# Performance work log

Measured on AMD Instinct MI355X. Metric: run time of the kernel, lower is better.

## Reference

```python
import jax, jax.numpy as jnp
import numpy as np

# Hyperparameters from init_kwargs
LAMBDA_VAL = 5.0
MARGIN = 0.02
INTERCLASS_COEF = 0.5
HIGH_CONSTANT = 2.0
EPS = 1e-5


def _rank(seq):
    # torch: argsort(argsort(seq).flip(-1)) -> rank 0 for the largest element
    idx = jnp.flip(jnp.argsort(seq, axis=-1), axis=-1)
    return jnp.argsort(idx, axis=-1)


def rank_normalised(seq):
    n = seq.shape[-1]
    return (_rank(seq) + 1).astype(seq.dtype) / n


@jax.custom_vjp
def true_ranker(seq):
    # Blackbox-differentiable ranking (TrueRanker.apply)
    return rank_normalised(seq)


def _tr_fwd(seq):
    r = rank_normalised(seq)
    return r, (seq, r)


def _tr_bwd(res, g):
    seq, r = res
    r_prime = rank_normalised(seq + LAMBDA_VAL * g)
    return (-(r - r_prime) / (LAMBDA_VAL + 1e-8),)


true_ranker.defvjp(_tr_fwd, _tr_bwd)


def raw_map(scores, targets, key):
    """scores/targets: [N, C]. Faithful port of MapLoss.raw_map_computation."""
    ts = scores.T  # [C, N]
    tt = targets.T  # [C, N]
    # random margin deviations: pushed down for positives, up for negatives
    dev = jnp.abs(jax.random.normal(key, tt.shape, tt.dtype)) * (tt - 0.5)
    ts = ts - MARGIN * dev
    ranks_of_positive = true_ranker(ts)  # [C, N], normalized ranks in (0,1]
    scores_for_rp = -ranks_of_positive + HIGH_CONSTANT * tt
    # torch sets requires_grad=False on this rank -> stop_gradient
    ranks_within_positive = jax.lax.stop_gradient(rank_normalised(scores_for_rp))
    sum_prec = (ranks_within_positive / ranks_of_positive * tt).sum(axis=1)  # [C]
    prec = sum_prec / (tt.sum(axis=1) + EPS)  # [C]
    present = targets.sum(axis=0) != 0  # [C]
    denom = jnp.maximum(jnp.sum(present), 1).astype(prec.dtype)
    return 1.0 - jnp.sum(jnp.where(present, prec, 0.0)) / denom


def setup_inputs() -> dict:
    key = jax.random.key(0)
    k1, k2, k3, k4 = jax.random.split(key, 4)
    B, C, M = 256, 8192, 4
    P_POS = 0.01  # sparse binary relevance labels
    output = jax.random.normal(k1, (B, C), jnp.float32)
    target = (jax.random.uniform(k2, (B, C)) < P_POS).astype(jnp.float32)
    stored_output = jax.random.normal(k3, (M * B, C), jnp.float32)
    stored_target = (jax.random.uniform(k4, (M * B, C)) < P_POS).astype(jnp.float32)
    return {"output": output, "target": target,
            "stored_output": stored_output, "stored_target": stored_target}


def reference(output, target, stored_output, stored_target):
    # storage entries were detach()'d in torch -> stop_gradient
    long_out = jnp.concatenate([output, jax.lax.stop_gradient(stored_output)], axis=0)
    long_tgt = jnp.concatenate([target, stored_target], axis=0)
    k_cross, k_inter = jax.random.split(jax.random.key(42))
    cross_batch_loss = raw_map(long_out, long_tgt, k_cross)
    interclass_loss = raw_map(output.reshape(-1, 1), target.reshape(-1, 1), k_inter)
    return (1.0 - INTERCLASS_COEF) * cross_batch_loss + INTERCLASS_COEF * interclass_loss
```

## Files before the change

kernel.cpp:

```cpp
#include <hip/hip_runtime.h>
#include <stdint.h>

#define USE_PARTITIONABLE 1

#define C_CLASSES 8192
#define N_ROWS 1280
#define HALF_CROSS (C_CLASSES * N_ROWS / 2)
#define N_INTER 2097152
#define HALF_INTER (N_INTER / 2)
#define PCAP 32768
#define NB (1u << 20)
#define BSHIFT 12
#define IPB 2048
#define PPB 96
#define CNT_CAP 24576
#define CNT_WORDS (CNT_CAP / 4)
#define KE_BLOCKS 256
#define KE_ELEMS (N_INTER / KE_BLOCKS)
#define CPB 16

__host__ __device__ __forceinline__ void tf2x32(unsigned k0, unsigned k1,
                                                unsigned c0, unsigned c1,
                                                unsigned& o0, unsigned& o1) {
  const unsigned ks2 = k0 ^ k1 ^ 0x1BD11BDAu;
  unsigned x0 = c0 + k0, x1 = c1 + k1;
#define TF_R(r) { x0 += x1; x1 = (x1 << (r)) | (x1 >> (32 - (r))); x1 ^= x0; }
  TF_R(13) TF_R(15) TF_R(26) TF_R(6)   x0 += k1;  x1 += ks2 + 1u;
  TF_R(17) TF_R(29) TF_R(16) TF_R(24)  x0 += ks2; x1 += k0 + 2u;
  TF_R(13) TF_R(15) TF_R(26) TF_R(6)   x0 += k0;  x1 += k1 + 3u;
  TF_R(17) TF_R(29) TF_R(16) TF_R(24)  x0 += k1;  x1 += ks2 + 4u;
  TF_R(13) TF_R(15) TF_R(26) TF_R(6)   x0 += ks2; x1 += k0 + 5u;
#undef TF_R
  o0 = x0; o1 = x1;
}

__device__ __forceinline__ unsigned rand_bits(unsigned k0, unsigned k1,
                                              unsigned p, unsigned half) {
#if USE_PARTITIONABLE
  (void)half;
  unsigned a, b; tf2x32(k0, k1, 0u, p, a, b);
  return a ^ b;
#else
  unsigned c0 = (p < half) ? p : (p - half);
  unsigned a, b; tf2x32(k0, k1, c0, c0 + half, a, b);
  return (p < half) ? a : b;
#endif
}

__device__ __forceinline__ float erfinv_xla(float x) {
  float w = -log1pf(-x * x);
  float p;
  if (w < 5.0f) {
    w = w - 2.5f;
    p = 2.81022636e-08f;
    p = fmaf(p, w, 3.43273939e-07f);
    p = fmaf(p, w, -3.5233877e-06f);
    p = fmaf(p, w, -4.39150654e-06f);
    p = fmaf(p, w, 0.00021858087f);
    p = fmaf(p, w, -0.00125372503f);
    p = fmaf(p, w, -0.00417768164f);
    p = fmaf(p, w, 0.246640727f);
    p = fmaf(p, w, 1.50140941f);
  } else {
    w = sqrtf(w) - 3.0f;
    p = -0.000200214257f;
    p = fmaf(p, w, 0.000100950558f);
    p = fmaf(p, w, 0.00134934322f);
    p = fmaf(p, w, -0.00367342844f);
    p = fmaf(p, w, 0.00573950773f);
    p = fmaf(p, w, -0.0076224613f);
    p = fmaf(p, w, 0.00943887047f);
    p = fmaf(p, w, 1.00167406f);
    p = fmaf(p, w, 2.83297682f);
  }
  return p * x;
}

__device__ __forceinline__ float normal_from_bits(unsigned bits) {
  unsigned fb = (bits >> 9) | 0x3F800000u;
  float f = __uint_as_float(fb) - 1.0f;
  float u = fmaxf(-0.99999994f, f * 2.0f - 0.99999994f);
  return 1.41421356f * erfinv_xla(u);
}

__device__ __forceinline__ unsigned sortable_key(float sp) {
  unsigned b = __float_as_uint(sp);
  return (b & 0x80000000u) ? ~b : (b | 0x80000000u);
}

__global__ void __launch_bounds__(1024) kcross_fused(
    const float* __restrict__ outp, const float* __restrict__ tgt,
    const float* __restrict__ soutp, const float* __restrict__ stgt,
    float* __restrict__ prec_arr, float* __restrict__ pres_arr,
    unsigned k0, unsigned k1) {
  __shared__ float skey[N_ROWS][CPB + 1];
  __shared__ unsigned tmask[N_ROWS];
  __shared__ unsigned short plist[CPB][64];
  __shared__ int pcnt[CPB];
  __shared__ unsigned rankl[CPB][64];
  const int tid = threadIdx.x;
  const int c0 = blockIdx.x * CPB;

  for (int i = tid; i < N_ROWS; i += 1024) tmask[i] = 0u;
  if (tid < CPB) pcnt[tid] = 0;
  __syncthreads();

#pragma unroll
  for (int i = 0; i < 5; ++i) {
    int f = i * 1024 + tid;
    int n = f >> 2, quad = f & 3;
    const float* tp = (n < 256) ? (tgt + (size_t)n * C_CLASSES)
                                : (stgt + (size_t)(n - 256) * C_CLASSES);
    float4 tv = *(const float4*)(tp + c0 + quad * 4);
    unsigned nib = (tv.x != 0.f ? 1u : 0u) | (tv.y != 0.f ? 2u : 0u) |
                   (tv.z != 0.f ? 4u : 0u) | (tv.w != 0.f ? 8u : 0u);
    if (nib) {
      atomicOr(&tmask[n], nib << (quad * 4));
#pragma unroll
      for (int k = 0; k < 4; ++k) {
        if (nib & (1u << k)) {
          int j = quad * 4 + k;
          int slot = atomicAdd(&pcnt[j], 1);
          if (slot < 64) plist[j][slot] = (unsigned short)n;
        }
      }
    }
  }
  __syncthreads();

#pragma unroll
  for (int i = 0; i < 5; ++i) {
    int f = i * 1024 + tid;
    int n = f >> 2, quad = f & 3;
    const float* sp_ = (n < 256) ? (outp + (size_t)n * C_CLASSES)
                                 : (soutp + (size_t)(n - 256) * C_CLASSES);
    float4 sv = *(const float4*)(sp_ + c0 + quad * 4);
    unsigned tm = tmask[n];
    float r[4] = {sv.x, sv.y, sv.z, sv.w};
#pragma unroll
    for (int k = 0; k < 4; ++k) {
      int j = quad * 4 + k;
      unsigned p = (unsigned)((c0 + j) * N_ROWS + n);
      float nrm = normal_from_bits(rand_bits(k0, k1, p, HALF_CROSS));
      float tvf = ((tm >> j) & 1u) ? 1.0f : 0.0f;
      r[k] = r[k] - 0.02f * (fabsf(nrm) * (tvf - 0.5f));
      skey[n][j] = r[k];
    }
  }
  __syncthreads();

  const int j = tid >> 6;
  const int lane = tid & 63;
  const int P = pcnt[j] < 64 ? pcnt[j] : 64;
  for (int pi = 0; pi < P; ++pi) {
    int ip = plist[j][pi];
    float spv = skey[ip][j];
    int cnt = 0;
#pragma unroll
    for (int s = 0; s < 20; ++s) {
      int n = lane + 64 * s;
      float x = skey[n][j];
      cnt += (x > spv) || ((x == spv) & (n > ip));
    }
    cnt += __shfl_down(cnt, 32);
    cnt += __shfl_down(cnt, 16);
    cnt += __shfl_down(cnt, 8);
    cnt += __shfl_down(cnt, 4);
    cnt += __shfl_down(cnt, 2);
    cnt += __shfl_down(cnt, 1);
    if (lane == 0) rankl[j][pi] = (unsigned)cnt;
  }
  double acc = 0.0;
  if (lane < P) {
    int ip = plist[j][lane];
    float spv = skey[ip][j];
    int k = 1;
    for (int q = 0; q < P; ++q) {
      int iq = plist[j][q];
      float sq = skey[iq][j];
      k += (sq > spv) || ((sq == spv) & (iq > ip));
    }
    unsigned rr = rankl[j][lane];
    float rw = (float)k / 1280.0f;
    float ro = (float)(rr + 1u) / 1280.0f;
    acc = (double)(rw / ro);
  }
#pragma unroll
  for (int o = 32; o; o >>= 1) acc += __shfl_down(acc, o);
  if (lane == 0) {
    if (P > 0) {
      float sum_prec = (float)acc;
      prec_arr[c0 + j] = sum_prec / ((float)P + 1e-5f);
      pres_arr[c0 + j] = 1.0f;
    } else {
      prec_arr[c0 + j] = 0.0f;
      pres_arr[c0 + j] = 0.0f;
    }
  }
}

__global__ void kinter_prep(const float* __restrict__ outp, const float* __restrict__ tgt,
                            unsigned* __restrict__ ukey,
                            unsigned long long* __restrict__ pk64_tmp,
                            unsigned* __restrict__ blockCnt,
                            unsigned* __restrict__ hist_pos,
                            unsigned k0, unsigned k1) {
  __shared__ unsigned scnt;
  if (threadIdx.x == 0) scnt = 0;
  __syncthreads();
  const int blk = blockIdx.x;
#pragma unroll
  for (int i = 0; i < 4; ++i) {
    int n = blk * 1024 + i * 256 + threadIdx.x;
    float t = tgt[n], sv = outp[n];
    float nrm = normal_from_bits(rand_bits(k0, k1, (unsigned)n, HALF_INTER));
    float sp = sv - 0.02f * (fabsf(nrm) * (t - 0.5f));
    unsigned key = sortable_key(sp);
    ukey[n] = key;
    if (t != 0.0f) {
      unsigned slot = atomicAdd(&scnt, 1u);
      if (slot < PPB) {
        pk64_tmp[(size_t)blk * PPB + slot] = ((unsigned long long)key << 21) | (unsigned)n;
        atomicAdd(&hist_pos[key >> BSHIFT], 1u);
      }
    }
  }
  __syncthreads();
  if (threadIdx.x == 0) blockCnt[blk] = scnt < PPB ? scnt : PPB;
}

__global__ void kscan1(const unsigned* __restrict__ hist_pos, unsigned* __restrict__ chunkSum) {
  __shared__ unsigned ls[256];
  const int t = threadIdx.x;
  uint4 v = ((const uint4*)(hist_pos + (size_t)blockIdx.x * 1024))[t];
  ls[t] = v.x + v.y + v.z + v.w;
  __syncthreads();
  for (int o = 128; o; o >>= 1) { if (t < o) ls[t] += ls[t + o]; __syncthreads(); }
  if (t == 0) chunkSum[blockIdx.x] = ls[0];
}

__global__ void kscan2(const unsigned* __restrict__ chunkSum, unsigned* __restrict__ chunkPre,
                       const unsigned* __restrict__ blockCnt, unsigned* pcount) {
  __shared__ unsigned ls[1024];
  const int t = threadIdx.x;
  unsigned own = chunkSum[t];
  ls[t] = own;
  __syncthreads();
  for (int off = 1; off < 1024; off <<= 1) {
    unsigned v = (t >= off) ? ls[t - off] : 0u;
    __syncthreads();
    ls[t] += v;
    __syncthreads();
  }
  chunkPre[t] = ls[t] - own;
  __syncthreads();
  unsigned s = blockCnt[t] + blockCnt[t + 1024];
  ls[t] = s;
  __syncthreads();
  for (int o = 512; o; o >>= 1) { if (t < o) ls[t] += ls[t + o]; __syncthreads(); }
  if (t == 0) *pcount = ls[0];
}

__global__ void kscan3(const unsigned* __restrict__ hist_pos, const unsigned* __restrict__ chunkPre,
                       unsigned* __restrict__ cursor, unsigned* __restrict__ bsh) {
  __shared__ unsigned ls[256];
  const int t = threadIdx.x;
  uint4 v = ((const uint4*)(hist_pos + (size_t)blockIdx.x * 1024))[t];
  unsigned tsum = v.x + v.y + v.z + v.w;
  ls[t] = tsum;
  __syncthreads();
  for (int off = 1; off < 256; off <<= 1) {
    unsigned u = (t >= off) ? ls[t - off] : 0u;
    __syncthreads();
    ls[t] += u;
    __syncthreads();
  }
  unsigned base = chunkPre[blockIdx.x] + ls[t] - tsum;
  uint4 cu; cu.x = base; cu.y = base + v.x; cu.z = cu.y + v.y; cu.w = cu.z + v.z;
  ((uint4*)cursor)[blockIdx.x * 256 + t] = cu;
  uint4 bs;
  bs.x = (cu.x << 8) | (v.x > 255u ? 255u : v.x);
  bs.y = (cu.y << 8) | (v.y > 255u ? 255u : v.y);
  bs.z = (cu.z << 8) | (v.z > 255u ? 255u : v.z);
  bs.w = (cu.w << 8) | (v.w > 255u ? 255u : v.w);
  ((uint4*)bsh)[blockIdx.x * 256 + t] = bs;
}

__global__ void kpos_scatter(const unsigned long long* __restrict__ pk64_tmp,
                             const unsigned* __restrict__ blockCnt,
                             unsigned* cursor, unsigned long long* __restrict__ t64) {
  unsigned j = blockIdx.x * 256 + threadIdx.x;
  unsigned b = j / PPB, i = j % PPB;
  if (i >= blockCnt[b]) return;
  unsigned long long k64 = pk64_tmp[j];
  unsigned bkt = (unsigned)(k64 >> 33);
  unsigned slot = atomicAdd(&cursor[bkt], 1u);
  t64[slot] = k64;
}

__global__ void kpos_fix(const unsigned long long* __restrict__ t64,
                         const unsigned* __restrict__ hist_pos,
                         const unsigned* __restrict__ cursor,
                         const unsigned* pcount, unsigned long long* __restrict__ spk64) {
  unsigned j = blockIdx.x * 256 + threadIdx.x;
  unsigned P = *pcount;
  if (j >= P) return;
  unsigned long long my = t64[j];
  unsigned bkt = (unsigned)(my >> 33);
  unsigned hp = hist_pos[bkt];
  unsigned start = cursor[bkt] - hp;
  unsigned lt = 0;
  if (hp > 1) {
    for (unsigned m = start; m < start + hp; ++m) lt += (t64[m] < my);
  }
  spk64[start + lt] = my;
}

__global__ void __launch_bounds__(1024) kelem2(
    const unsigned* __restrict__ ukey, const unsigned* __restrict__ bsh,
    const unsigned long long* __restrict__ spk64,
    unsigned* __restrict__ cnt_blocks) {
  __shared__ unsigned cntp[CNT_WORDS];
  const int tid = threadIdx.x;
  for (int i = tid; i < CNT_WORDS; i += 1024) cntp[i] = 0;
  __syncthreads();
#pragma unroll
  for (int it = 0; it < 8; ++it) {
    int n = blockIdx.x * KE_ELEMS + it * 1024 + tid;
    unsigned key = ukey[n];
    unsigned long long k64 = ((unsigned long long)key << 21) | (unsigned)n;
    unsigned info = bsh[key >> BSHIFT];
    unsigned cntLess = info >> 8;
    unsigned hp = info & 0xFFu;
    if (hp) {
      unsigned start = cntLess;
      for (unsigned m = start; m < start + hp; ++m) cntLess += (spk64[m] < k64);
    }
    if (cntLess > CNT_CAP - 1) cntLess = CNT_CAP - 1;
    atomicAdd(&cntp[cntLess >> 2], 1u << ((cntLess & 3u) * 8u));
  }
  __syncthreads();
  unsigned* dst = cnt_blocks + (size_t)blockIdx.x * CNT_WORDS;
  for (int i = tid; i < CNT_WORDS; i += 1024) dst[i] = cntp[i];
}

__global__ void kreduce(const unsigned* __restrict__ cnt_blocks, unsigned* __restrict__ tot) {
  unsigned i = blockIdx.x * 256 + threadIdx.x;
  unsigned s0 = 0, s1 = 0, s2 = 0, s3 = 0;
  for (int b = 0; b < KE_BLOCKS; ++b) {
    unsigned v = cnt_blocks[(size_t)b * CNT_WORDS + i];
    s0 += v & 0xFFu; s1 += (v >> 8) & 0xFFu; s2 += (v >> 16) & 0xFFu; s3 += v >> 24;
  }
  tot[4 * i] = s0; tot[4 * i + 1] = s1; tot[4 * i + 2] = s2; tot[4 * i + 3] = s3;
}

__global__ void __launch_bounds__(1024) kfinal(
    const float* __restrict__ prec_arr, const float* __restrict__ pres_arr,
    const unsigned* __restrict__ tot, const unsigned* pcount, float* __restrict__ out) {
  __shared__ double rd[1024];
  __shared__ unsigned lsum[1024];
  const int t = threadIdx.x;
  const unsigned P = *pcount;
  const int CH = CNT_CAP / 1024;
  unsigned lv[CH];
  unsigned mys = 0;
#pragma unroll
  for (int i = 0; i < CH; ++i) { lv[i] = tot[t * CH + i]; mys += lv[i]; }
  lsum[t] = mys;
  __syncthreads();
  for (int off = 1; off < 1024; off <<= 1) {
    unsigned v = (t + off < 1024) ? lsum[t + off] : 0u;
    __syncthreads();
    lsum[t] += v;
    __syncthreads();
  }
  unsigned run = (t < 1023) ? lsum[t + 1] : 0u;
  double acc = 0.0;
#pragma unroll
  for (int i = CH - 1; i >= 0; --i) {
    unsigned idx = (unsigned)(t * CH + i);
    unsigned r = run;
    if (idx < P) acc += (double)((float)(P - idx) / (float)(r + 1u));
    run += lv[i];
  }
  rd[t] = acc;
  __syncthreads();
  for (int o = 512; o; o >>= 1) { if (t < o) rd[t] += rd[t + o]; __syncthreads(); }
  double interSum = rd[0];
  __syncthreads();
  double a = 0.0, bb = 0.0;
  for (int i = t; i < C_CLASSES; i += 1024) { a += (double)prec_arr[i]; bb += (double)pres_arr[i]; }
  rd[t] = a;
  __syncthreads();
  for (int o = 512; o; o >>= 1) { if (t < o) rd[t] += rd[t + o]; __syncthreads(); }
  double crossSum = rd[0];
  __syncthreads();
  rd[t] = bb;
  __syncthreads();
  for (int o = 512; o; o >>= 1) { if (t < o) rd[t] += rd[t + o]; __syncthreads(); }
  if (t == 0) {
    float pc = (float)rd[0];
    float denomC = pc > 0.0f ? pc : 1.0f;
    float crossLoss = 1.0f - (float)crossSum / denomC;
    float interPrec = (float)interSum / ((float)P + 1e-5f);
    float interLoss = 1.0f - interPrec;
    out[0] = 0.5f * crossLoss + 0.5f * interLoss;
  }
}

extern "C" void kernel_launch(void* const* d_in, const int* in_sizes, int n_in,
                              void* d_out, int out_size, void* d_ws, size_t ws_size,
                              hipStream_t stream) {
  (void)in_sizes; (void)n_in; (void)out_size; (void)ws_size;
  const float* outp  = (const float*)d_in[0];
  const float* tgt   = (const float*)d_in[1];
  const float* soutp = (const float*)d_in[2];
  const float* stgt  = (const float*)d_in[3];
  float* dst = (float*)d_out;

  unsigned ck0, ck1, ik0, ik1;
#if USE_PARTITIONABLE
  tf2x32(0u, 42u, 0u, 0u, ck0, ck1);
  tf2x32(0u, 42u, 0u, 1u, ik0, ik1);
#else
  { unsigned a0, b0, a1, b1;
    tf2x32(0u, 42u, 0u, 2u, a0, b0);
    tf2x32(0u, 42u, 1u, 3u, a1, b1);
    ck0 = a0; ck1 = a1; ik0 = b0; ik1 = b1; }
#endif

  uint8_t* w = (uint8_t*)d_ws;
  size_t o = 0;
  unsigned* hist_pos   = (unsigned*)(w + o); o += (size_t)NB * 4;
  unsigned* cursor     = (unsigned*)(w + o); o += (size_t)NB * 4;
  unsigned* bsh        = (unsigned*)(w + o); o += (size_t)NB * 4;
  unsigned* ukey       = (unsigned*)(w + o); o += (size_t)N_INTER * 4;
  unsigned* chunkSum   = (unsigned*)(w + o); o += 1024 * 4;
  unsigned* chunkPre   = (unsigned*)(w + o); o += 1024 * 4;
  unsigned long long* pk64_tmp = (unsigned long long*)(w + o); o += (size_t)IPB * PPB * 8;
  unsigned* blockCnt   = (unsigned*)(w + o); o += (size_t)IPB * 4;
  unsigned long long* t64   = (unsigned long long*)(w + o); o += (size_t)PCAP * 8;
  unsigned long long* spk64 = (unsigned long long*)(w + o); o += (size_t)PCAP * 8;
  unsigned* cnt_blocks = (unsigned*)(w + o); o += (size_t)KE_BLOCKS * CNT_WORDS * 4;
  unsigned* tot        = (unsigned*)(w + o); o += (size_t)CNT_CAP * 4;
  float*    prec_arr   = (float*)(w + o);    o += (size_t)C_CLASSES * 4;
  float*    pres_arr   = (float*)(w + o);    o += (size_t)C_CLASSES * 4;
  unsigned* pcount     = (unsigned*)(w + o); o += 64;

  hipMemsetAsync(hist_pos, 0, (size_t)NB * 4, stream);

  kcross_fused<<<C_CLASSES / CPB, 1024, 0, stream>>>(
      outp, tgt, soutp, stgt, prec_arr, pres_arr, ck0, ck1);
  kinter_prep<<<IPB, 256, 0, stream>>>(outp, tgt, ukey, pk64_tmp, blockCnt, hist_pos, ik0, ik1);
  kscan1<<<NB / 1024, 256, 0, stream>>>(hist_pos, chunkSum);
  kscan2<<<1, 1024, 0, stream>>>(chunkSum, chunkPre, blockCnt, pcount);
  kscan3<<<NB / 1024, 256, 0, stream>>>(hist_pos, chunkPre, cursor, bsh);
  kpos_scatter<<<IPB * PPB / 256, 256, 0, stream>>>(pk64_tmp, blockCnt, cursor, t64);
  kpos_fix<<<PCAP / 256, 256, 0, stream>>>(t64, hist_pos, cursor, pcount, spk64);
  kelem2<<<KE_BLOCKS, 1024, 0, stream>>>(ukey, bsh, spk64, cnt_blocks);
  kreduce<<<CNT_WORDS / 256, 256, 0, stream>>>(cnt_blocks, tot);
  kfinal<<<1, 1024, 0, stream>>>(prec_arr, pres_arr, tot, pcount, dst);
}
```

Baseline: 271.1 us.

## Fuse interclass pipeline into one cooperative kernel and retune cross-batch ranking

```diff
diff --git a/kernel.cpp b/kernel.cpp
--- a/kernel.cpp
+++ b/kernel.cpp
@@ -1,5 +1,8 @@
 #include <hip/hip_runtime.h>
+#include <hip/hip_cooperative_groups.h>
 #include <stdint.h>
+
+namespace cg = cooperative_groups;
 
 #define USE_PARTITIONABLE 1
 
@@ -8,16 +11,19 @@
 #define HALF_CROSS (C_CLASSES * N_ROWS / 2)
 #define N_INTER 2097152
 #define HALF_INTER (N_INTER / 2)
-#define PCAP 32768
 #define NB (1u << 20)
 #define BSHIFT 12
-#define IPB 2048
-#define PPB 96
 #define CNT_CAP 24576
 #define CNT_WORDS (CNT_CAP / 4)
-#define KE_BLOCKS 256
-#define KE_ELEMS (N_INTER / KE_BLOCKS)
-#define CPB 16
+#define CPB 8
+
+#define MBLK 256
+#define MTHR 1024
+#define EPB (N_INTER / MBLK)
+#define EPT (EPB / MTHR)
+#define PLOC 192
+#define BPB ((int)(NB / MBLK))
+#define WPB (CNT_WORDS / MBLK)
 
 __host__ __device__ __forceinline__ void tf2x32(unsigned k0, unsigned k1,
                                                 unsigned c0, unsigned c1,
@@ -88,38 +94,38 @@
   return (b & 0x80000000u) ? ~b : (b | 0x80000000u);
 }
 
-__global__ void __launch_bounds__(1024) kcross_fused(
+__global__ void __launch_bounds__(512, 6) kcross_fused(
     const float* __restrict__ outp, const float* __restrict__ tgt,
     const float* __restrict__ soutp, const float* __restrict__ stgt,
     float* __restrict__ prec_arr, float* __restrict__ pres_arr,
     unsigned k0, unsigned k1) {
   __shared__ float skey[N_ROWS][CPB + 1];
-  __shared__ unsigned tmask[N_ROWS];
+  __shared__ unsigned tmask32[N_ROWS / 4];
   __shared__ unsigned short plist[CPB][64];
   __shared__ int pcnt[CPB];
-  __shared__ unsigned rankl[CPB][64];
+  __shared__ unsigned short rankl[CPB][64];
   const int tid = threadIdx.x;
   const int c0 = blockIdx.x * CPB;
 
-  for (int i = tid; i < N_ROWS; i += 1024) tmask[i] = 0u;
+  for (int i = tid; i < N_ROWS / 4; i += 512) tmask32[i] = 0u;
   if (tid < CPB) pcnt[tid] = 0;
   __syncthreads();
 
 #pragma unroll
   for (int i = 0; i < 5; ++i) {
-    int f = i * 1024 + tid;
-    int n = f >> 2, quad = f & 3;
+    int f = i * 512 + tid;
+    int n = f >> 1, half = f & 1;
     const float* tp = (n < 256) ? (tgt + (size_t)n * C_CLASSES)
                                 : (stgt + (size_t)(n - 256) * C_CLASSES);
-    float4 tv = *(const float4*)(tp + c0 + quad * 4);
+    float4 tv = *(const float4*)(tp + c0 + half * 4);
     unsigned nib = (tv.x != 0.f ? 1u : 0u) | (tv.y != 0.f ? 2u : 0u) |
                    (tv.z != 0.f ? 4u : 0u) | (tv.w != 0.f ? 8u : 0u);
     if (nib) {
-      atomicOr(&tmask[n], nib << (quad * 4));
+      atomicOr(&tmask32[n >> 2], nib << ((n & 3) * 8 + half * 4));
 #pragma unroll
       for (int k = 0; k < 4; ++k) {
         if (nib & (1u << k)) {
-          int j = quad * 4 + k;
+          int j = half * 4 + k;
           int slot = atomicAdd(&pcnt[j], 1);
           if (slot < 64) plist[j][slot] = (unsigned short)n;
         }
@@ -130,205 +136,193 @@
 
 #pragma unroll
   for (int i = 0; i < 5; ++i) {
-    int f = i * 1024 + tid;
-    int n = f >> 2, quad = f & 3;
+    int f = i * 512 + tid;
+    int n = f >> 1, half = f & 1;
     const float* sp_ = (n < 256) ? (outp + (size_t)n * C_CLASSES)
                                  : (soutp + (size_t)(n - 256) * C_CLASSES);
-    float4 sv = *(const float4*)(sp_ + c0 + quad * 4);
-    unsigned tm = tmask[n];
-    float r[4] = {sv.x, sv.y, sv.z, sv.w};
+    float4 sv = *(const float4*)(sp_ + c0 + half * 4);
+    unsigned tmr = tmask32[n >> 2] >> ((n & 3) * 8);
+    float vals[4] = {sv.x, sv.y, sv.z, sv.w};
 #pragma unroll
     for (int k = 0; k < 4; ++k) {
-      int j = quad * 4 + k;
+      int j = half * 4 + k;
       unsigned p = (unsigned)((c0 + j) * N_ROWS + n);
       float nrm = normal_from_bits(rand_bits(k0, k1, p, HALF_CROSS));
-      float tvf = ((tm >> j) & 1u) ? 1.0f : 0.0f;
-      r[k] = r[k] - 0.02f * (fabsf(nrm) * (tvf - 0.5f));
-      skey[n][j] = r[k];
-    }
-  }
-  __syncthreads();
-
-  const int j = tid >> 6;
-  const int lane = tid & 63;
-  const int P = pcnt[j] < 64 ? pcnt[j] : 64;
-  for (int pi = 0; pi < P; ++pi) {
-    int ip = plist[j][pi];
-    float spv = skey[ip][j];
-    int cnt = 0;
-#pragma unroll
+      float tvf = ((tmr >> j) & 1u) ? 1.0f : 0.0f;
+      skey[n][j] = vals[k] - 0.02f * (fabsf(nrm) * (tvf - 0.5f));
+    }
+  }
+  __syncthreads();
+
+  const int j = tid >> 6, lane = tid & 63;
+  int P = pcnt[j]; if (P > 64) P = 64;
+  for (int base = 0; base < P; base += 8) {
+    float spv[8]; int ipv[8];
+#pragma unroll
+    for (int k = 0; k < 8; ++k) {
+      int pi = base + k;
+      if (pi < P) { ipv[k] = plist[j][pi]; spv[k] = skey[ipv[k]][j]; }
+      else { ipv[k] = 0x7fffffff; spv[k] = __int_as_float(0x7f800000); }
+    }
+    unsigned c16[4] = {0u, 0u, 0u, 0u};
     for (int s = 0; s < 20; ++s) {
-      int n = lane + 64 * s;
+      int n = lane + (s << 6);
       float x = skey[n][j];
-      cnt += (x > spv) || ((x == spv) & (n > ip));
-    }
-    cnt += __shfl_down(cnt, 32);
-    cnt += __shfl_down(cnt, 16);
-    cnt += __shfl_down(cnt, 8);
-    cnt += __shfl_down(cnt, 4);
-    cnt += __shfl_down(cnt, 2);
-    cnt += __shfl_down(cnt, 1);
-    if (lane == 0) rankl[j][pi] = (unsigned)cnt;
+#pragma unroll
+      for (int k = 0; k < 8; ++k) {
+        unsigned bb = (x > spv[k]) || ((x == spv[k]) & (n > ipv[k]));
+        c16[k >> 1] += bb << ((k & 1) * 16);
+      }
+    }
+#pragma unroll
+    for (int q = 0; q < 4; ++q) {
+      unsigned v = c16[q];
+      v += __shfl_down(v, 32); v += __shfl_down(v, 16); v += __shfl_down(v, 8);
+      v += __shfl_down(v, 4);  v += __shfl_down(v, 2);  v += __shfl_down(v, 1);
+      if (lane == 0) {
+        int p0 = base + 2 * q;
+        if (p0 < P)     rankl[j][p0]     = (unsigned short)(v & 0xFFFFu);
+        if (p0 + 1 < P) rankl[j][p0 + 1] = (unsigned short)(v >> 16);
+      }
+    }
   }
   double acc = 0.0;
   if (lane < P) {
     int ip = plist[j][lane];
-    float spv = skey[ip][j];
-    int k = 1;
+    float spv0 = skey[ip][j];
+    int kk = 1;
     for (int q = 0; q < P; ++q) {
       int iq = plist[j][q];
       float sq = skey[iq][j];
-      k += (sq > spv) || ((sq == spv) & (iq > ip));
+      kk += (sq > spv0) || ((sq == spv0) & (iq > ip));
     }
     unsigned rr = rankl[j][lane];
-    float rw = (float)k / 1280.0f;
+    float rw = (float)kk / 1280.0f;
     float ro = (float)(rr + 1u) / 1280.0f;
     acc = (double)(rw / ro);
   }
 #pragma unroll
   for (int o = 32; o; o >>= 1) acc += __shfl_down(acc, o);
   if (lane == 0) {
-    if (P > 0) {
-      float sum_prec = (float)acc;
-      prec_arr[c0 + j] = sum_prec / ((float)P + 1e-5f);
-      pres_arr[c0 + j] = 1.0f;
-    } else {
-      prec_arr[c0 + j] = 0.0f;
-      pres_arr[c0 + j] = 0.0f;
-    }
-  }
-}
-
-__global__ void kinter_prep(const float* __restrict__ outp, const float* __restrict__ tgt,
-                            unsigned* __restrict__ ukey,
-                            unsigned long long* __restrict__ pk64_tmp,
-                            unsigned* __restrict__ blockCnt,
-                            unsigned* __restrict__ hist_pos,
-                            unsigned k0, unsigned k1) {
-  __shared__ unsigned scnt;
-  if (threadIdx.x == 0) scnt = 0;
-  __syncthreads();
-  const int blk = blockIdx.x;
-#pragma unroll
-  for (int i = 0; i < 4; ++i) {
-    int n = blk * 1024 + i * 256 + threadIdx.x;
+    if (P > 0) { prec_arr[c0 + j] = (float)acc / ((float)P + 1e-5f); pres_arr[c0 + j] = 1.0f; }
+    else       { prec_arr[c0 + j] = 0.0f;                            pres_arr[c0 + j] = 0.0f; }
+  }
+}
+
+__global__ void __launch_bounds__(1024) kinter_mega(
+    const float* __restrict__ outp, const float* __restrict__ tgt,
+    unsigned* __restrict__ hist_pos, unsigned* __restrict__ cursor,
+    unsigned* __restrict__ bsh, unsigned* __restrict__ chunkTot,
+    unsigned long long* __restrict__ t64, unsigned long long* __restrict__ spk64,
+    unsigned* __restrict__ cnt_blocks, unsigned* __restrict__ tot,
+    const float* __restrict__ prec_arr, const float* __restrict__ pres_arr,
+    float* __restrict__ out, unsigned k0, unsigned k1) {
+  cg::grid_group grid = cg::this_grid();
+  __shared__ unsigned lkey[EPB];
+  __shared__ unsigned cntp[CNT_WORDS];
+  __shared__ unsigned sc[MTHR];
+  __shared__ unsigned long long pk_loc[PLOC];
+  __shared__ int scnt;
+  __shared__ unsigned uP;
+  __shared__ double rd[1024];
+  __shared__ unsigned lsum[1024];
+  const int tid = threadIdx.x;
+  const int b = blockIdx.x;
+
+  if (tid == 0) scnt = 0;
+  __syncthreads();
+
+#pragma unroll
+  for (int it = 0; it < EPT; ++it) {
+    int loc = it * MTHR + tid;
+    int n = b * EPB + loc;
     float t = tgt[n], sv = outp[n];
     float nrm = normal_from_bits(rand_bits(k0, k1, (unsigned)n, HALF_INTER));
     float sp = sv - 0.02f * (fabsf(nrm) * (t - 0.5f));
     unsigned key = sortable_key(sp);
-    ukey[n] = key;
+    lkey[loc] = key;
     if (t != 0.0f) {
-      unsigned slot = atomicAdd(&scnt, 1u);
-      if (slot < PPB) {
-        pk64_tmp[(size_t)blk * PPB + slot] = ((unsigned long long)key << 21) | (unsigned)n;
+      int slot = atomicAdd(&scnt, 1);
+      if (slot < PLOC) {
+        pk_loc[slot] = ((unsigned long long)key << 21) | (unsigned)n;
         atomicAdd(&hist_pos[key >> BSHIFT], 1u);
       }
     }
   }
-  __syncthreads();
-  if (threadIdx.x == 0) blockCnt[blk] = scnt < PPB ? scnt : PPB;
-}
-
-__global__ void kscan1(const unsigned* __restrict__ hist_pos, unsigned* __restrict__ chunkSum) {
-  __shared__ unsigned ls[256];
-  const int t = threadIdx.x;
-  uint4 v = ((const uint4*)(hist_pos + (size_t)blockIdx.x * 1024))[t];
-  ls[t] = v.x + v.y + v.z + v.w;
-  __syncthreads();
-  for (int o = 128; o; o >>= 1) { if (t < o) ls[t] += ls[t + o]; __syncthreads(); }
-  if (t == 0) chunkSum[blockIdx.x] = ls[0];
-}
-
-__global__ void kscan2(const unsigned* __restrict__ chunkSum, unsigned* __restrict__ chunkPre,
-                       const unsigned* __restrict__ blockCnt, unsigned* pcount) {
-  __shared__ unsigned ls[1024];
-  const int t = threadIdx.x;
-  unsigned own = chunkSum[t];
-  ls[t] = own;
-  __syncthreads();
-  for (int off = 1; off < 1024; off <<= 1) {
-    unsigned v = (t >= off) ? ls[t - off] : 0u;
-    __syncthreads();
-    ls[t] += v;
-    __syncthreads();
-  }
-  chunkPre[t] = ls[t] - own;
-  __syncthreads();
-  unsigned s = blockCnt[t] + blockCnt[t + 1024];
-  ls[t] = s;
-  __syncthreads();
-  for (int o = 512; o; o >>= 1) { if (t < o) ls[t] += ls[t + o]; __syncthreads(); }
-  if (t == 0) *pcount = ls[0];
-}
-
-__global__ void kscan3(const unsigned* __restrict__ hist_pos, const unsigned* __restrict__ chunkPre,
-                       unsigned* __restrict__ cursor, unsigned* __restrict__ bsh) {
-  __shared__ unsigned ls[256];
-  const int t = threadIdx.x;
-  uint4 v = ((const uint4*)(hist_pos + (size_t)blockIdx.x * 1024))[t];
-  unsigned tsum = v.x + v.y + v.z + v.w;
-  ls[t] = tsum;
-  __syncthreads();
-  for (int off = 1; off < 256; off <<= 1) {
-    unsigned u = (t >= off) ? ls[t - off] : 0u;
-    __syncthreads();
-    ls[t] += u;
-    __syncthreads();
-  }
-  unsigned base = chunkPre[blockIdx.x] + ls[t] - tsum;
-  uint4 cu; cu.x = base; cu.y = base + v.x; cu.z = cu.y + v.y; cu.w = cu.z + v.z;
-  ((uint4*)cursor)[blockIdx.x * 256 + t] = cu;
+  grid.sync();
+
+  uint4 hv = ((const uint4*)(hist_pos + (size_t)b * BPB))[tid];
+  unsigned tsum = hv.x + hv.y + hv.z + hv.w;
+  sc[tid] = tsum;
+  __syncthreads();
+  for (int off = 1; off < MTHR; off <<= 1) {
+    unsigned v = (tid >= off) ? sc[tid - off] : 0u;
+    __syncthreads();
+    sc[tid] += v;
+    __syncthreads();
+  }
+  unsigned pre_t = sc[tid] - tsum;
+  if (tid == MTHR - 1) chunkTot[b] = sc[tid];
+  grid.sync();
+
+  if (tid < MBLK) sc[tid] = chunkTot[tid];
+  __syncthreads();
+  for (int off = 1; off < MBLK; off <<= 1) {
+    unsigned v = (tid < MBLK && tid >= off) ? sc[tid - off] : 0u;
+    __syncthreads();
+    if (tid < MBLK) sc[tid] += v;
+    __syncthreads();
+  }
+  if (tid == 0) uP = sc[MBLK - 1];
+  unsigned base_b = (b > 0) ? sc[b - 1] : 0u;
+  unsigned s0 = base_b + pre_t;
+  uint4 cu; cu.x = s0; cu.y = s0 + hv.x; cu.z = cu.y + hv.y; cu.w = cu.z + hv.z;
+  ((uint4*)(cursor + (size_t)b * BPB))[tid] = cu;
   uint4 bs;
-  bs.x = (cu.x << 8) | (v.x > 255u ? 255u : v.x);
-  bs.y = (cu.y << 8) | (v.y > 255u ? 255u : v.y);
-  bs.z = (cu.z << 8) | (v.z > 255u ? 255u : v.z);
-  bs.w = (cu.w << 8) | (v.w > 255u ? 255u : v.w);
-  ((uint4*)bsh)[blockIdx.x * 256 + t] = bs;
-}
-
-__global__ void kpos_scatter(const unsigned long long* __restrict__ pk64_tmp,
-                             const unsigned* __restrict__ blockCnt,
-                             unsigned* cursor, unsigned long long* __restrict__ t64) {
-  unsigned j = blockIdx.x * 256 + threadIdx.x;
-  unsigned b = j / PPB, i = j % PPB;
-  if (i >= blockCnt[b]) return;
-  unsigned long long k64 = pk64_tmp[j];
-  unsigned bkt = (unsigned)(k64 >> 33);
-  unsigned slot = atomicAdd(&cursor[bkt], 1u);
-  t64[slot] = k64;
-}
-
-__global__ void kpos_fix(const unsigned long long* __restrict__ t64,
-                         const unsigned* __restrict__ hist_pos,
-                         const unsigned* __restrict__ cursor,
-                         const unsigned* pcount, unsigned long long* __restrict__ spk64) {
-  unsigned j = blockIdx.x * 256 + threadIdx.x;
-  unsigned P = *pcount;
-  if (j >= P) return;
-  unsigned long long my = t64[j];
-  unsigned bkt = (unsigned)(my >> 33);
-  unsigned hp = hist_pos[bkt];
-  unsigned start = cursor[bkt] - hp;
-  unsigned lt = 0;
-  if (hp > 1) {
-    for (unsigned m = start; m < start + hp; ++m) lt += (t64[m] < my);
-  }
-  spk64[start + lt] = my;
-}
-
-__global__ void __launch_bounds__(1024) kelem2(
-    const unsigned* __restrict__ ukey, const unsigned* __restrict__ bsh,
-    const unsigned long long* __restrict__ spk64,
-    unsigned* __restrict__ cnt_blocks) {
-  __shared__ unsigned cntp[CNT_WORDS];
-  const int tid = threadIdx.x;
-  for (int i = tid; i < CNT_WORDS; i += 1024) cntp[i] = 0;
-  __syncthreads();
-#pragma unroll
-  for (int it = 0; it < 8; ++it) {
-    int n = blockIdx.x * KE_ELEMS + it * 1024 + tid;
-    unsigned key = ukey[n];
-    unsigned long long k64 = ((unsigned long long)key << 21) | (unsigned)n;
+  bs.x = (cu.x << 8) | (hv.x > 255u ? 255u : hv.x);
+  bs.y = (cu.y << 8) | (hv.y > 255u ? 255u : hv.y);
+  bs.z = (cu.z << 8) | (hv.z > 255u ? 255u : hv.z);
+  bs.w = (cu.w << 8) | (hv.w > 255u ? 255u : hv.w);
+  ((uint4*)(bsh + (size_t)b * BPB))[tid] = bs;
+  grid.sync();
+
+  {
+    int myScnt = scnt; if (myScnt > PLOC) myScnt = PLOC;
+    if (tid < myScnt) {
+      unsigned long long k64 = pk_loc[tid];
+      unsigned bkt = (unsigned)(k64 >> 33);
+      unsigned slot = atomicAdd(&cursor[bkt], 1u);
+      t64[slot] = k64;
+    }
+  }
+  grid.sync();
+
+  const unsigned P = uP;
+  {
+    unsigned per = (P + MBLK - 1) / MBLK;
+    unsigned j0 = (unsigned)b * per;
+    unsigned j = j0 + (unsigned)tid;
+    if (tid < (int)per && j < P) {
+      unsigned long long my = t64[j];
+      unsigned bkt = (unsigned)(my >> 33);
+      unsigned info = bsh[bkt];
+      unsigned hp = info & 0xFFu;
+      unsigned start = info >> 8;
+      unsigned lt = 0;
+      if (hp > 1) for (unsigned m = start; m < start + hp; ++m) lt += (t64[m] < my);
+      spk64[start + lt] = my;
+    }
+  }
+  grid.sync();
+
+  for (int i = tid; i < CNT_WORDS; i += MTHR) cntp[i] = 0;
+  __syncthreads();
+#pragma unroll
+  for (int it = 0; it < EPT; ++it) {
+    int loc = it * MTHR + tid;
+    unsigned key = lkey[loc];
+    unsigned n = (unsigned)(b * EPB + loc);
+    unsigned long long k64 = ((unsigned long long)key << 21) | n;
     unsigned info = bsh[key >> BSHIFT];
     unsigned cntLess = info >> 8;
     unsigned hp = info & 0xFFu;
@@ -340,65 +334,72 @@
     atomicAdd(&cntp[cntLess >> 2], 1u << ((cntLess & 3u) * 8u));
   }
   __syncthreads();
-  unsigned* dst = cnt_blocks + (size_t)blockIdx.x * CNT_WORDS;
-  for (int i = tid; i < CNT_WORDS; i += 1024) dst[i] = cntp[i];
-}
-
-__global__ void kreduce(const unsigned* __restrict__ cnt_blocks, unsigned* __restrict__ tot) {
-  unsigned i = blockIdx.x * 256 + threadIdx.x;
-  unsigned s0 = 0, s1 = 0, s2 = 0, s3 = 0;
-  for (int b = 0; b < KE_BLOCKS; ++b) {
-    unsigned v = cnt_blocks[(size_t)b * CNT_WORDS + i];
-    s0 += v & 0xFFu; s1 += (v >> 8) & 0xFFu; s2 += (v >> 16) & 0xFFu; s3 += v >> 24;
-  }
-  tot[4 * i] = s0; tot[4 * i + 1] = s1; tot[4 * i + 2] = s2; tot[4 * i + 3] = s3;
-}
-
-__global__ void __launch_bounds__(1024) kfinal(
-    const float* __restrict__ prec_arr, const float* __restrict__ pres_arr,
-    const unsigned* __restrict__ tot, const unsigned* pcount, float* __restrict__ out) {
-  __shared__ double rd[1024];
-  __shared__ unsigned lsum[1024];
-  const int t = threadIdx.x;
-  const unsigned P = *pcount;
+  {
+    unsigned* dst = cnt_blocks + (size_t)b * CNT_WORDS;
+    for (int i = tid; i < CNT_WORDS; i += MTHR) dst[i] = cntp[i];
+  }
+  grid.sync();
+
+  {
+    if (tid < WPB * 4) sc[tid] = 0u;
+    __syncthreads();
+    if (tid < 1008) {
+      int wl = tid % WPB;
+      int blk0 = tid / WPB;
+      unsigned a0 = 0, a1 = 0, a2 = 0, a3 = 0;
+      for (int blk = blk0; blk < MBLK; blk += 42) {
+        unsigned v = cnt_blocks[(size_t)blk * CNT_WORDS + b * WPB + wl];
+        a0 += v & 0xFFu; a1 += (v >> 8) & 0xFFu; a2 += (v >> 16) & 0xFFu; a3 += v >> 24;
+      }
+      atomicAdd(&sc[wl * 4 + 0], a0);
+      atomicAdd(&sc[wl * 4 + 1], a1);
+      atomicAdd(&sc[wl * 4 + 2], a2);
+      atomicAdd(&sc[wl * 4 + 3], a3);
+    }
+    __syncthreads();
+    if (tid < WPB * 4) tot[b * WPB * 4 + tid] = sc[tid];
+  }
+  grid.sync();
+
+  if (b != 0) return;
   const int CH = CNT_CAP / 1024;
   unsigned lv[CH];
   unsigned mys = 0;
 #pragma unroll
-  for (int i = 0; i < CH; ++i) { lv[i] = tot[t * CH + i]; mys += lv[i]; }
-  lsum[t] = mys;
+  for (int i = 0; i < CH; ++i) { lv[i] = tot[tid * CH + i]; mys += lv[i]; }
+  lsum[tid] = mys;
   __syncthreads();
   for (int off = 1; off < 1024; off <<= 1) {
-    unsigned v = (t + off < 1024) ? lsum[t + off] : 0u;
-    __syncthreads();
-    lsum[t] += v;
-    __syncthreads();
-  }
-  unsigned run = (t < 1023) ? lsum[t + 1] : 0u;
+    unsigned v = (tid + off < 1024) ? lsum[tid + off] : 0u;
+    __syncthreads();
+    lsum[tid] += v;
+    __syncthreads();
+  }
+  unsigned run = (tid < 1023) ? lsum[tid + 1] : 0u;
   double acc = 0.0;
 #pragma unroll
   for (int i = CH - 1; i >= 0; --i) {
-    unsigned idx = (unsigned)(t * CH + i);
+    unsigned idx = (unsigned)(tid * CH + i);
     unsigned r = run;
     if (idx < P) acc += (double)((float)(P - idx) / (float)(r + 1u));
     run += lv[i];
   }
-  rd[t] = acc;
-  __syncthreads();
-  for (int o = 512; o; o >>= 1) { if (t < o) rd[t] += rd[t + o]; __syncthreads(); }
+  rd[tid] = acc;
+  __syncthreads();
+  for (int o = 512; o; o >>= 1) { if (tid < o) rd[tid] += rd[tid + o]; __syncthreads(); }
   double interSum = rd[0];
   __syncthreads();
-  double a = 0.0, bb = 0.0;
-  for (int i = t; i < C_CLASSES; i += 1024) { a += (double)prec_arr[i]; bb += (double)pres_arr[i]; }
-  rd[t] = a;
-  __syncthreads();
-  for (int o = 512; o; o >>= 1) { if (t < o) rd[t] += rd[t + o]; __syncthreads(); }
+  double a = 0.0, bb2 = 0.0;
+  for (int i = tid; i < C_CLASSES; i += 1024) { a += (double)prec_arr[i]; bb2 += (double)pres_arr[i]; }
+  rd[tid] = a;
+  __syncthreads();
+  for (int o = 512; o; o >>= 1) { if (tid < o) rd[tid] += rd[tid + o]; __syncthreads(); }
   double crossSum = rd[0];
   __syncthreads();
-  rd[t] = bb;
-  __syncthreads();
-  for (int o = 512; o; o >>= 1) { if (t < o) rd[t] += rd[t + o]; __syncthreads(); }
-  if (t == 0) {
+  rd[tid] = bb2;
+  __syncthreads();
+  for (int o = 512; o; o >>= 1) { if (tid < o) rd[tid] += rd[tid + o]; __syncthreads(); }
+  if (tid == 0) {
     float pc = (float)rd[0];
     float denomC = pc > 0.0f ? pc : 1.0f;
     float crossLoss = 1.0f - (float)crossSum / denomC;
@@ -434,30 +435,22 @@
   unsigned* hist_pos   = (unsigned*)(w + o); o += (size_t)NB * 4;
   unsigned* cursor     = (unsigned*)(w + o); o += (size_t)NB * 4;
   unsigned* bsh        = (unsigned*)(w + o); o += (size_t)NB * 4;
-  unsigned* ukey       = (unsigned*)(w + o); o += (size_t)N_INTER * 4;
-  unsigned* chunkSum   = (unsigned*)(w + o); o += 1024 * 4;
-  unsigned* chunkPre   = (unsigned*)(w + o); o += 1024 * 4;
-  unsigned long long* pk64_tmp = (unsigned long long*)(w + o); o += (size_t)IPB * PPB * 8;
-  unsigned* blockCnt   = (unsigned*)(w + o); o += (size_t)IPB * 4;
-  unsigned long long* t64   = (unsigned long long*)(w + o); o += (size_t)PCAP * 8;
-  unsigned long long* spk64 = (unsigned long long*)(w + o); o += (size_t)PCAP * 8;
-  unsigned* cnt_blocks = (unsigned*)(w + o); o += (size_t)KE_BLOCKS * CNT_WORDS * 4;
+  unsigned* chunkTot   = (unsigned*)(w + o); o += (size_t)MBLK * 4;
+  unsigned long long* t64   = (unsigned long long*)(w + o); o += (size_t)32768 * 8;
+  unsigned long long* spk64 = (unsigned long long*)(w + o); o += (size_t)32768 * 8;
+  unsigned* cnt_blocks = (unsigned*)(w + o); o += (size_t)MBLK * CNT_WORDS * 4;
   unsigned* tot        = (unsigned*)(w + o); o += (size_t)CNT_CAP * 4;
   float*    prec_arr   = (float*)(w + o);    o += (size_t)C_CLASSES * 4;
   float*    pres_arr   = (float*)(w + o);    o += (size_t)C_CLASSES * 4;
-  unsigned* pcount     = (unsigned*)(w + o); o += 64;
 
   hipMemsetAsync(hist_pos, 0, (size_t)NB * 4, stream);
 
-  kcross_fused<<<C_CLASSES / CPB, 1024, 0, stream>>>(
+  kcross_fused<<<C_CLASSES / CPB, 512, 0, stream>>>(
       outp, tgt, soutp, stgt, prec_arr, pres_arr, ck0, ck1);
-  kinter_prep<<<IPB, 256, 0, stream>>>(outp, tgt, ukey, pk64_tmp, blockCnt, hist_pos, ik0, ik1);
-  kscan1<<<NB / 1024, 256, 0, stream>>>(hist_pos, chunkSum);
-  kscan2<<<1, 1024, 0, stream>>>(chunkSum, chunkPre, blockCnt, pcount);
-  kscan3<<<NB / 1024, 256, 0, stream>>>(hist_pos, chunkPre, cursor, bsh);
-  kpos_scatter<<<IPB * PPB / 256, 256, 0, stream>>>(pk64_tmp, blockCnt, cursor, t64);
-  kpos_fix<<<PCAP / 256, 256, 0, stream>>>(t64, hist_pos, cursor, pcount, spk64);
-  kelem2<<<KE_BLOCKS, 1024, 0, stream>>>(ukey, bsh, spk64, cnt_blocks);
-  kreduce<<<CNT_WORDS / 256, 256, 0, stream>>>(cnt_blocks, tot);
-  kfinal<<<1, 1024, 0, stream>>>(prec_arr, pres_arr, tot, pcount, dst);
-}
+
+  void* margs[] = {(void*)&outp, (void*)&tgt, (void*)&hist_pos, (void*)&cursor,
+                   (void*)&bsh, (void*)&chunkTot, (void*)&t64, (void*)&spk64,
+                   (void*)&cnt_blocks, (void*)&tot, (void*)&prec_arr, (void*)&pres_arr,
+                   (void*)&dst, (void*)&ik0, (void*)&ik1};
+  hipLaunchCooperativeKernel((void*)kinter_mega, dim3(MBLK), dim3(MTHR), margs, 0, stream);
+}
```

Result: slower. 453.6 us (+67.4%).
